# Optimization experiments

Measured on AMD Instinct MI355X. Metric: run time of the kernel, lower is better.

The kernel has to match this reference:

```python
import jax, jax.numpy as jnp
import numpy as np

N = 50000
E = 1600000
IN_CH = 128
HEADS = 4
C = 32  # out_channels // heads
NEG_SLOPE = 0.2


def setup_inputs() -> dict:
    key = jax.random.key(0)
    k1, k2, k3, k4, k5, k6 = jax.random.split(key, 6)
    x = jax.random.normal(k1, (N, IN_CH), dtype=jnp.float32)
    edge_index = jax.random.randint(k2, (2, E), 0, N, dtype=jnp.int64)
    # GATConv params (PyG): lin weight, att_src, att_dst, bias
    s = 1.0 / np.sqrt(IN_CH)
    W = jax.random.uniform(k3, (IN_CH, HEADS * C), dtype=jnp.float32, minval=-s, maxval=s)
    att_src = jax.random.normal(k4, (HEADS, C), dtype=jnp.float32) * 0.1
    att_dst = jax.random.normal(k5, (HEADS, C), dtype=jnp.float32) * 0.1
    bias = jnp.zeros((HEADS * C,), dtype=jnp.float32)
    return {"x": x, "edge_index": edge_index, "W": W, "att_src": att_src, "att_dst": att_dst, "bias": bias}


def reference(x, edge_index, W, att_src, att_dst, bias):
    n = x.shape[0]
    # add self-loops (PyG default add_self_loops=True)
    loop = jnp.arange(n, dtype=edge_index.dtype)
    src = jnp.concatenate([edge_index[0], loop])
    dst = jnp.concatenate([edge_index[1], loop])
    # project: [N, H, C]
    h = (x @ W).reshape(n, HEADS, C)
    # per-node attention logits: [N, H]
    a_src = jnp.einsum("nhc,hc->nh", h, att_src)
    a_dst = jnp.einsum("nhc,hc->nh", h, att_dst)
    # per-edge logits with leaky relu: [E', H]
    alpha = a_src[src] + a_dst[dst]
    alpha = jnp.where(alpha > 0, alpha, NEG_SLOPE * alpha)
    # segment softmax over incoming edges of each destination node
    amax = jax.ops.segment_max(alpha, dst, num_segments=n)  # [N, H]
    ex = jnp.exp(alpha - amax[dst])
    denom = jax.ops.segment_sum(ex, dst, num_segments=n)  # [N, H]
    coef = ex / denom[dst]  # [E', H]
    # weighted scatter-aggregate of source features
    msg = h[src] * coef[:, :, None]  # [E', H, C]
    out = jax.ops.segment_sum(msg, dst, num_segments=n)  # [N, H, C]
    return out.reshape(n, HEADS * C) + bias
```

## Files before the change

### kernel.cpp

```cpp
#include <hip/hip_runtime.h>
#include <hip/hip_bf16.h>
#include <hip/hip_fp16.h>

#define HEADS 4
#define C 32
#define OUTCH 128
#define INCH 128
#define NEG_SLOPE 0.2f

#define BKT 64
#define BKT_BITS 6
#define SBL 256

struct alignas(8) h2x2 { __half2 a, b; };

__global__ __launch_bounds__(256) void k_hist(const int* __restrict__ dst,
                                              int* __restrict__ hist,
                                              int E, int NB, int chunk) {
    __shared__ int lh[1024];
    int blk = blockIdx.x;
    for (int i = threadIdx.x; i < NB; i += 256) lh[i] = 0;
    __syncthreads();
    int beg = blk * chunk, end = min(E, beg + chunk);
    for (int e = beg + threadIdx.x; e < end; e += 256)
        atomicAdd(&lh[dst[e] >> BKT_BITS], 1);
    __syncthreads();
    int cm = (blk & 7) * (SBL / 8) + (blk >> 3);
    for (int b = threadIdx.x; b < NB; b += 256) hist[b * SBL + cm] = lh[b];
}

__global__ __launch_bounds__(1024) void k_scan1(const int* __restrict__ v,
                                                int* __restrict__ incl,
                                                int* __restrict__ bsum, int n) {
    __shared__ int sm[1024];
    int t = threadIdx.x;
    int g = blockIdx.x * 1024 + t;
    int x = (g < n) ? v[g] : 0;
    sm[t] = x;
    __syncthreads();
    for (int off = 1; off < 1024; off <<= 1) {
        int add = (t >= off) ? sm[t - off] : 0;
        __syncthreads();
        sm[t] += add;
        __syncthreads();
    }
    if (g < n) incl[g] = sm[t];
    if (t == 1023) bsum[blockIdx.x] = sm[t];
}

__global__ __launch_bounds__(1024) void k_scan2(int* __restrict__ bsum, int nb) {
    __shared__ int sm[1024];
    int t = threadIdx.x;
    int x = (t < nb) ? bsum[t] : 0;
    sm[t] = x;
    __syncthreads();
    for (int off = 1; off < 1024; off <<= 1) {
        int add = (t >= off) ? sm[t - off] : 0;
        __syncthreads();
        sm[t] += add;
        __syncthreads();
    }
    if (t < nb) bsum[t] = sm[t] - x;
}

__global__ __launch_bounds__(1024) void k_scan3(const int* __restrict__ incl,
                                                const int* __restrict__ bsumx,
                                                const int* __restrict__ v,
                                                int* __restrict__ sOff, int n) {
    int g = blockIdx.x * 1024 + threadIdx.x;
    if (g < n) {
        int inc = incl[g] + bsumx[blockIdx.x];
        sOff[g] = inc - v[g];
        if (g == n - 1) sOff[n] = inc;
    }
}

__global__ __launch_bounds__(256) void k_scatter(const int* __restrict__ src,
                                                 const int* __restrict__ dst,
                                                 const int* __restrict__ sOff,
                                                 unsigned int* __restrict__ pairs,
                                                 int E, int NB, int chunk) {
    __shared__ int cur[1024];
    int blk = blockIdx.x;
    int cm = (blk & 7) * (SBL / 8) + (blk >> 3);
    for (int b = threadIdx.x; b < NB; b += 256) cur[b] = sOff[b * SBL + cm];
    __syncthreads();
    int beg = blk * chunk, end = min(E, beg + chunk);
    for (int e = beg + threadIdx.x; e < end; e += 256) {
        int d = dst[e];
        int b = d >> BKT_BITS;
        int pos = atomicAdd(&cur[b], 1);
        pairs[pos] = ((unsigned)(d & (BKT - 1)) << 26) | (unsigned)src[e];
    }
}

__global__ __launch_bounds__(256) void k_bfill(const unsigned int* __restrict__ pairs,
                                               const int* __restrict__ sOff,
                                               int* __restrict__ offs,
                                               int* __restrict__ deg,
                                               int* __restrict__ srcl, int n) {
    __shared__ int hist64[64];
    __shared__ int cur[64];
    int b = blockIdx.x;
    int t = threadIdx.x;
    int start = sOff[b * SBL];
    int end   = sOff[(b + 1) * SBL];
    if (t < 64) hist64[t] = 0;
    __syncthreads();
    for (int i = start + t; i < end; i += 256)
        atomicAdd(&hist64[pairs[i] >> 26], 1);
    __syncthreads();
    if (t < 64) {
        int v = hist64[t];
        int incl = v;
        for (int off = 1; off < 64; off <<= 1) {
            int u = __shfl_up(incl, off);
            if (t >= off) incl += u;
        }
        int excl = incl - v;
        cur[t] = start + excl;
        int node = (b << BKT_BITS) + t;
        if (node < n) { offs[node] = start + excl; deg[node] = v; }
    }
    __syncthreads();
    for (int i = start + t; i < end; i += 256) {
        unsigned p = pairs[i];
        int pos = atomicAdd(&cur[p >> 26], 1);
        srcl[pos] = p & 0x3FFFFFF;
    }
}

__global__ __launch_bounds__(256) void k_gemm(const float* __restrict__ x,
                                              const float* __restrict__ W,
                                              const float* __restrict__ att_src,
                                              const float* __restrict__ att_dst,
                                              __half* __restrict__ h16,
                                              float* __restrict__ a_src,
                                              float* __restrict__ a_dst, int n) {
    __shared__ float xs[64][128];
    int t = threadIdx.x;
    int rowBase = blockIdx.x * 64;
    for (int i = t; i < 64 * 32; i += 256) {
        int r = i >> 5, c4 = i & 31;
        float4 v = {0.f, 0.f, 0.f, 0.f};
        if (rowBase + r < n)
            v = *(const float4*)(x + (size_t)(rowBase + r) * INCH + c4 * 4);
        *(float4*)&xs[r][c4 * 4] = v;
    }
    __syncthreads();

    int colg = t & 31;
    int rowg = t >> 5;
    float acc[8][4] = {};
    const float4* W4 = (const float4*)W;
    for (int k = 0; k < 128; ++k) {
        float4 w = W4[k * 32 + colg];
#pragma unroll
        for (int i = 0; i < 8; ++i) {
            float xv = xs[rowg * 8 + i][k];
            acc[i][0] = fmaf(xv, w.x, acc[i][0]);
            acc[i][1] = fmaf(xv, w.y, acc[i][1]);
            acc[i][2] = fmaf(xv, w.z, acc[i][2]);
            acc[i][3] = fmaf(xv, w.w, acc[i][3]);
        }
    }

    int head = colg >> 3;
    float as4[4], ad4[4];
#pragma unroll
    for (int c = 0; c < 4; ++c) {
        int within = (colg & 7) * 4 + c;
        as4[c] = att_src[head * C + within];
        ad4[c] = att_dst[head * C + within];
    }
#pragma unroll
    for (int i = 0; i < 8; ++i) {
        int r = rowBase + rowg * 8 + i;
        if (r < n) {
            h2x2 pk;
            pk.a = __floats2half2_rn(acc[i][0], acc[i][1]);
            pk.b = __floats2half2_rn(acc[i][2], acc[i][3]);
            *(h2x2*)(h16 + (size_t)r * OUTCH + colg * 4) = pk;
        }
        float ps = acc[i][0] * as4[0] + acc[i][1] * as4[1] +
                   acc[i][2] * as4[2] + acc[i][3] * as4[3];
        float pd = acc[i][0] * ad4[0] + acc[i][1] * ad4[1] +
                   acc[i][2] * ad4[2] + acc[i][3] * ad4[3];
        ps += __shfl_xor(ps, 1); ps += __shfl_xor(ps, 2); ps += __shfl_xor(ps, 4);
        pd += __shfl_xor(pd, 1); pd += __shfl_xor(pd, 2); pd += __shfl_xor(pd, 4);
        if ((colg & 7) == 0 && r < n) {
            a_src[(size_t)r * 4 + head] = ps;
            a_dst[(size_t)r * 4 + head] = pd;
        }
    }
}

__global__ __launch_bounds__(256) void k_aggr(const __half* __restrict__ h16,
                                              const float* __restrict__ a_src,
                                              const float* __restrict__ a_dst,
                                              const int* __restrict__ offs,
                                              const int* __restrict__ deg,
                                              const int* __restrict__ srcl,
                                              const float* __restrict__ bias,
                                              float* __restrict__ out, int n) {
    int w = (blockIdx.x * 256 + threadIdx.x) >> 6;
    if (w >= n) return;
    int lane = threadIdx.x & 63;
    int head = lane >> 4;
    int ch = lane << 1;
    const __half2* H2 = (const __half2*)h16;

    float adst = a_dst[(size_t)w * 4 + head];

    float al = a_src[(size_t)w * 4 + head] + adst;
    al = al > 0.f ? al : NEG_SLOPE * al;
    float ex = __expf(al);
    float2 hv = __half22float2(H2[(size_t)w * 64 + lane]);
    float f0 = ex * hv.x, f1 = ex * hv.y, den = ex;

    int start = offs[w], d = deg[w];
    int j = 0;
    for (; j + 4 <= d; j += 4) {
        int s0 = srcl[start + j];
        int s1 = srcl[start + j + 1];
        int s2 = srcl[start + j + 2];
        int s3 = srcl[start + j + 3];
        float b0 = a_src[(size_t)s0 * 4 + head] + adst;
        float b1 = a_src[(size_t)s1 * 4 + head] + adst;
        float b2 = a_src[(size_t)s2 * 4 + head] + adst;
        float b3 = a_src[(size_t)s3 * 4 + head] + adst;
        __half2 g0 = H2[(size_t)s0 * 64 + lane];
        __half2 g1 = H2[(size_t)s1 * 64 + lane];
        __half2 g2 = H2[(size_t)s2 * 64 + lane];
        __half2 g3 = H2[(size_t)s3 * 64 + lane];
        b0 = b0 > 0.f ? b0 : NEG_SLOPE * b0;
        b1 = b1 > 0.f ? b1 : NEG_SLOPE * b1;
        b2 = b2 > 0.f ? b2 : NEG_SLOPE * b2;
        b3 = b3 > 0.f ? b3 : NEG_SLOPE * b3;
        float e0 = __expf(b0), e1 = __expf(b1), e2 = __expf(b2), e3 = __expf(b3);
        den += (e0 + e1) + (e2 + e3);
        float2 G0 = __half22float2(g0);
        float2 G1 = __half22float2(g1);
        float2 G2 = __half22float2(g2);
        float2 G3 = __half22float2(g3);
        f0 = fmaf(e0, G0.x, f0); f1 = fmaf(e0, G0.y, f1);
        f0 = fmaf(e1, G1.x, f0); f1 = fmaf(e1, G1.y, f1);
        f0 = fmaf(e2, G2.x, f0); f1 = fmaf(e2, G2.y, f1);
        f0 = fmaf(e3, G3.x, f0); f1 = fmaf(e3, G3.y, f1);
    }
    for (; j < d; ++j) {
        int s0 = srcl[start + j];
        float b0 = a_src[(size_t)s0 * 4 + head] + adst;
        __half2 g0 = H2[(size_t)s0 * 64 + lane];
        b0 = b0 > 0.f ? b0 : NEG_SLOPE * b0;
        float e0 = __expf(b0);
        den += e0;
        float2 G0 = __half22float2(g0);
        f0 = fmaf(e0, G0.x, f0); f1 = fmaf(e0, G0.y, f1);
    }

    float inv = 1.0f / den;
    float2 bv = *(const float2*)(bias + ch);
    float2 o;
    o.x = f0 * inv + bv.x;
    o.y = f1 * inv + bv.y;
    *(float2*)(out + (size_t)w * OUTCH + ch) = o;
}

extern "C" void kernel_launch(void* const* d_in, const int* in_sizes, int n_in,
                              void* d_out, int out_size, void* d_ws, size_t ws_size,
                              hipStream_t stream) {
    const float* x       = (const float*)d_in[0];
    const int*   edge    = (const int*)d_in[1];
    const float* W       = (const float*)d_in[2];
    const float* att_src = (const float*)d_in[3];
    const float* att_dst = (const float*)d_in[4];
    const float* bias    = (const float*)d_in[5];
    float* out = (float*)d_out;

    const int N = in_sizes[0] / INCH;
    const int E = in_sizes[1] / 2;
    const int* esrc = edge;
    const int* edst = edge + E;

    const int NB = (N + BKT - 1) >> BKT_BITS;
    const int n2 = NB * SBL;
    const int chunk = (E + SBL - 1) / SBL;

    auto align = [](size_t v) { return (v + 255) & ~(size_t)255; };
    char* p = (char*)d_ws;
    __half* h16   = (__half*)p; p += align((size_t)N * OUTCH * 2);
    float* a_src  = (float*)p; p += align((size_t)N * 4 * 4);
    float* a_dst  = (float*)p; p += align((size_t)N * 4 * 4);
    int*   hist   = (int*)p;   p += align((size_t)n2 * 4);
    int*   incl   = (int*)p;   p += align((size_t)(n2 + 1) * 4);
    int*   sOff   = (int*)p;   p += align((size_t)(n2 + 1) * 4);
    int*   bsum   = (int*)p;   p += align(1024 * 4);
    int*   offs   = (int*)p;   p += align((size_t)N * 4);
    int*   deg    = (int*)p;   p += align((size_t)N * 4);
    unsigned int* pairs = (unsigned int*)p; p += align((size_t)E * 4);
    int*   srcl   = (int*)p;   p += align((size_t)E * 4);

    const int SCB = (n2 + 1023) / 1024;

    k_hist<<<SBL, 256, 0, stream>>>(edst, hist, E, NB, chunk);
    k_scan1<<<SCB, 1024, 0, stream>>>(hist, incl, bsum, n2);
    k_scan2<<<1, 1024, 0, stream>>>(bsum, SCB);
    k_scan3<<<SCB, 1024, 0, stream>>>(incl, bsum, hist, sOff, n2);
    k_scatter<<<SBL, 256, 0, stream>>>(esrc, edst, sOff, pairs, E, NB, chunk);
    k_bfill<<<NB, 256, 0, stream>>>(pairs, sOff, offs, deg, srcl, N);

    k_gemm<<<(N + 63) / 64, 256, 0, stream>>>(x, W, att_src, att_dst, h16, a_src, a_dst, N);
    k_aggr<<<(N + 3) / 4, 256, 0, stream>>>(h16, a_src, a_dst, offs, deg, srcl, bias, out, N);
}
```

Before: 229.7 us.

## Precompute per-edge exp logits in CSR fill kernel and reuse in aggregation

Moves the projection GEMM ahead of the CSR build so the bucket-fill kernel can compute each edge's leaky-ReLU and exp for all four heads and store them as fp16 alongside the sorted source list. The aggregation kernel then reads a precomputed fp16 weight per edge instead of gathering a_src and evaluating exp per head lane. This removes redundant exp work and the scattered a_src gathers in the hot loop. In exchange it adds an 8-byte-per-edge write and read, and loses precision by rounding the exp values to half, which also risks overflow for large logits since no max is subtracted.

```diff
diff --git a/kernel.cpp b/kernel.cpp
--- a/kernel.cpp
+++ b/kernel.cpp
@@ -94,18 +94,27 @@
     }
 }
 
-__global__ __launch_bounds__(256) void k_bfill(const unsigned int* __restrict__ pairs,
-                                               const int* __restrict__ sOff,
-                                               int* __restrict__ offs,
-                                               int* __restrict__ deg,
-                                               int* __restrict__ srcl, int n) {
+__global__ __launch_bounds__(256) void k_bfillex(const unsigned int* __restrict__ pairs,
+                                                 const int* __restrict__ sOff,
+                                                 const float* __restrict__ a_src,
+                                                 const float* __restrict__ a_dst,
+                                                 int* __restrict__ offs,
+                                                 int* __restrict__ deg,
+                                                 int* __restrict__ srcl,
+                                                 h2x2* __restrict__ ex, int n) {
     __shared__ int hist64[64];
     __shared__ int cur[64];
+    __shared__ float ad[64][4];
     int b = blockIdx.x;
     int t = threadIdx.x;
+    int n0 = b << BKT_BITS;
     int start = sOff[b * SBL];
     int end   = sOff[(b + 1) * SBL];
     if (t < 64) hist64[t] = 0;
+    if (t < 256) {
+        int node = n0 + (t >> 2);
+        ad[t >> 2][t & 3] = (node < n) ? a_dst[(size_t)node * 4 + (t & 3)] : 0.f;
+    }
     __syncthreads();
     for (int i = start + t; i < end; i += 256)
         atomicAdd(&hist64[pairs[i] >> 26], 1);
@@ -119,14 +128,29 @@
         }
         int excl = incl - v;
         cur[t] = start + excl;
-        int node = (b << BKT_BITS) + t;
+        int node = n0 + t;
         if (node < n) { offs[node] = start + excl; deg[node] = v; }
     }
     __syncthreads();
     for (int i = start + t; i < end; i += 256) {
         unsigned p = pairs[i];
-        int pos = atomicAdd(&cur[p >> 26], 1);
-        srcl[pos] = p & 0x3FFFFFF;
+        int local = p >> 26;
+        int s = p & 0x3FFFFFF;
+        int pos = atomicAdd(&cur[local], 1);
+        srcl[pos] = s;
+        float4 as = *(const float4*)(a_src + (size_t)s * 4);
+        float b0 = as.x + ad[local][0];
+        float b1 = as.y + ad[local][1];
+        float b2 = as.z + ad[local][2];
+        float b3 = as.w + ad[local][3];
+        b0 = fmaxf(b0, NEG_SLOPE * b0);
+        b1 = fmaxf(b1, NEG_SLOPE * b1);
+        b2 = fmaxf(b2, NEG_SLOPE * b2);
+        b3 = fmaxf(b3, NEG_SLOPE * b3);
+        h2x2 pk;
+        pk.a = __floats2half2_rn(__expf(b0), __expf(b1));
+        pk.b = __floats2half2_rn(__expf(b2), __expf(b3));
+        ex[pos] = pk;
     }
 }
 
@@ -196,6 +220,7 @@
 }
 
 __global__ __launch_bounds__(256) void k_aggr(const __half* __restrict__ h16,
+                                              const __half* __restrict__ ex,
                                               const float* __restrict__ a_src,
                                               const float* __restrict__ a_dst,
                                               const int* __restrict__ offs,
@@ -210,34 +235,28 @@
     int ch = lane << 1;
     const __half2* H2 = (const __half2*)h16;
 
-    float adst = a_dst[(size_t)w * 4 + head];
-
-    float al = a_src[(size_t)w * 4 + head] + adst;
-    al = al > 0.f ? al : NEG_SLOPE * al;
-    float ex = __expf(al);
+    float al = a_src[(size_t)w * 4 + head] + a_dst[(size_t)w * 4 + head];
+    al = fmaxf(al, NEG_SLOPE * al);
+    float exs = __expf(al);
     float2 hv = __half22float2(H2[(size_t)w * 64 + lane]);
-    float f0 = ex * hv.x, f1 = ex * hv.y, den = ex;
+    float f0 = exs * hv.x, f1 = exs * hv.y, den = exs;
 
     int start = offs[w], d = deg[w];
     int j = 0;
     for (; j + 4 <= d; j += 4) {
-        int s0 = srcl[start + j];
-        int s1 = srcl[start + j + 1];
-        int s2 = srcl[start + j + 2];
-        int s3 = srcl[start + j + 3];
-        float b0 = a_src[(size_t)s0 * 4 + head] + adst;
-        float b1 = a_src[(size_t)s1 * 4 + head] + adst;
-        float b2 = a_src[(size_t)s2 * 4 + head] + adst;
-        float b3 = a_src[(size_t)s3 * 4 + head] + adst;
+        size_t p = (size_t)(start + j);
+        int s0 = srcl[p];
+        int s1 = srcl[p + 1];
+        int s2 = srcl[p + 2];
+        int s3 = srcl[p + 3];
+        float e0 = __half2float(ex[p * 4 + head]);
+        float e1 = __half2float(ex[(p + 1) * 4 + head]);
+        float e2 = __half2float(ex[(p + 2) * 4 + head]);
+        float e3 = __half2float(ex[(p + 3) * 4 + head]);
         __half2 g0 = H2[(size_t)s0 * 64 + lane];
         __half2 g1 = H2[(size_t)s1 * 64 + lane];
         __half2 g2 = H2[(size_t)s2 * 64 + lane];
         __half2 g3 = H2[(size_t)s3 * 64 + lane];
-        b0 = b0 > 0.f ? b0 : NEG_SLOPE * b0;
-        b1 = b1 > 0.f ? b1 : NEG_SLOPE * b1;
-        b2 = b2 > 0.f ? b2 : NEG_SLOPE * b2;
-        b3 = b3 > 0.f ? b3 : NEG_SLOPE * b3;
-        float e0 = __expf(b0), e1 = __expf(b1), e2 = __expf(b2), e3 = __expf(b3);
         den += (e0 + e1) + (e2 + e3);
         float2 G0 = __half22float2(g0);
         float2 G1 = __half22float2(g1);
@@ -249,11 +268,10 @@
         f0 = fmaf(e3, G3.x, f0); f1 = fmaf(e3, G3.y, f1);
     }
     for (; j < d; ++j) {
-        int s0 = srcl[start + j];
-        float b0 = a_src[(size_t)s0 * 4 + head] + adst;
+        size_t p = (size_t)(start + j);
+        int s0 = srcl[p];
+        float e0 = __half2float(ex[p * 4 + head]);
         __half2 g0 = H2[(size_t)s0 * 64 + lane];
-        b0 = b0 > 0.f ? b0 : NEG_SLOPE * b0;
-        float e0 = __expf(b0);
         den += e0;
         float2 G0 = __half22float2(g0);
         f0 = fmaf(e0, G0.x, f0); f1 = fmaf(e0, G0.y, f1);
@@ -300,16 +318,19 @@
     int*   deg    = (int*)p;   p += align((size_t)N * 4);
     unsigned int* pairs = (unsigned int*)p; p += align((size_t)E * 4);
     int*   srcl   = (int*)p;   p += align((size_t)E * 4);
+    h2x2*  ex     = (h2x2*)p;  p += align((size_t)E * 8);
 
     const int SCB = (n2 + 1023) / 1024;
+
+    k_gemm<<<(N + 63) / 64, 256, 0, stream>>>(x, W, att_src, att_dst, h16, a_src, a_dst, N);
 
     k_hist<<<SBL, 256, 0, stream>>>(edst, hist, E, NB, chunk);
     k_scan1<<<SCB, 1024, 0, stream>>>(hist, incl, bsum, n2);
     k_scan2<<<1, 1024, 0, stream>>>(bsum, SCB);
     k_scan3<<<SCB, 1024, 0, stream>>>(incl, bsum, hist, sOff, n2);
     k_scatter<<<SBL, 256, 0, stream>>>(esrc, edst, sOff, pairs, E, NB, chunk);
-    k_bfill<<<NB, 256, 0, stream>>>(pairs, sOff, offs, deg, srcl, N);
-
-    k_gemm<<<(N + 63) / 64, 256, 0, stream>>>(x, W, att_src, att_dst, h16, a_src, a_dst, N);
-    k_aggr<<<(N + 3) / 4, 256, 0, stream>>>(h16, a_src, a_dst, offs, deg, srcl, bias, out, N);
-}
+    k_bfillex<<<NB, 256, 0, stream>>>(pairs, sOff, a_src, a_dst, offs, deg, srcl, ex, N);
+
+    k_aggr<<<(N + 3) / 4, 256, 0, stream>>>(h16, (const __half*)ex, a_src, a_dst,
+                                            offs, deg, srcl, bias, out, N);
+}
```

Result: slower. 235.7 us (+2.6%).
